# Performance work log

Measured on AMD Instinct MI355X. Metric: run time of the kernel, lower is better.

## Reference

```python
import jax, jax.numpy as jnp
import numpy as np

D_MODEL = 1280
N_HEADS = 16
DEPTH = D_MODEL // N_HEADS  # 80
NEG_BIG = -10000.0


def setup_inputs() -> dict:
    key = jax.random.key(0)
    ks = jax.random.split(key, 12)
    B, S = 2, 2048
    std = 1.0 / np.sqrt(D_MODEL)
    inp = {
        "v": jax.random.normal(ks[0], (B, S, D_MODEL), jnp.float32),
        "k": jax.random.normal(ks[1], (B, S, D_MODEL), jnp.float32),
        "q": jax.random.normal(ks[2], (B, S, D_MODEL), jnp.float32),
        # causal mask: 1.0 on strictly-upper triangle (future positions)
        "mask": jnp.triu(jnp.ones((S, S), jnp.float32), k=1),
        "Wq_w": jax.random.normal(ks[3], (D_MODEL, D_MODEL), jnp.float32) * std,
        "Wq_b": jnp.zeros((D_MODEL,), jnp.float32),
        "Wk_w": jax.random.normal(ks[4], (D_MODEL, D_MODEL), jnp.float32) * std,
        "Wk_b": jnp.zeros((D_MODEL,), jnp.float32),
        "Wv_w": jax.random.normal(ks[5], (D_MODEL, D_MODEL), jnp.float32) * std,
        "Wv_b": jnp.zeros((D_MODEL,), jnp.float32),
        "dense_w": jax.random.normal(ks[6], (D_MODEL, D_MODEL), jnp.float32) * std,
        "dense_b": jnp.zeros((D_MODEL,), jnp.float32),
    }
    return inp


def _split_heads(x, B):
    # [B, S, D] -> [B, H, S, depth]
    return x.reshape(B, -1, N_HEADS, DEPTH).transpose(0, 2, 1, 3)


def reference(v, k, q, mask, Wq_w, Wq_b, Wk_w, Wk_b, Wv_w, Wv_b, dense_w, dense_b):
    B = q.shape[0]
    # torch Linear: y = x @ W.T + b
    qh = _split_heads(q @ Wq_w.T + Wq_b, B)
    kh = _split_heads(k @ Wk_w.T + Wk_b, B)
    vh = _split_heads(v @ Wv_w.T + Wv_b, B)

    scale = 1.0 / np.sqrt(DEPTH)
    logits = jnp.einsum("bhqd,bhkd->bhqk", qh, kh) * scale  # [B,H,S,S]
    nd, ns = logits.shape[-2], logits.shape[-1]
    logits = logits + mask[ns - nd:ns, :ns] * NEG_BIG
    attn = jax.nn.softmax(logits, axis=-1)
    out = jnp.einsum("bhqk,bhkd->bhqd", attn, vh)  # [B,H,S,depth]
    out = out.transpose(0, 2, 1, 3).reshape(B, -1, D_MODEL)
    out = out @ dense_w.T + dense_b
    return out, attn
```

## Files before the change

### kernel.cpp

```cpp
#include <hip/hip_runtime.h>
#include <hip/hip_bf16.h>

typedef short frag8 __attribute__((ext_vector_type(8)));
typedef float facc4 __attribute__((ext_vector_type(4)));
typedef float f32x4 __attribute__((ext_vector_type(4)));
typedef unsigned short ushort_t;
typedef unsigned int uint_t;

#define DEV static __device__ __forceinline__

DEV ushort_t f2bf(float f) {
  uint_t u = __float_as_uint(f);
  u += 0x7fffu + ((u >> 16) & 1u);
  return (ushort_t)(u >> 16);
}
DEV uint_t cvt_pk(float lo, float hi) {
  uint_t r;
  asm("v_cvt_pk_bf16_f32 %0, %1, %2" : "=v"(r) : "v"(lo), "v"(hi));
  return r;
}
DEV frag8 pack8(float4 a, float4 b) {
  union { frag8 f; uint4 u; } u_;
  u_.u.x = cvt_pk(a.x, a.y); u_.u.y = cvt_pk(a.z, a.w);
  u_.u.z = cvt_pk(b.x, b.y); u_.u.w = cvt_pk(b.z, b.w);
  return u_.f;
}

constexpr int B_ = 2, S_ = 2048, H_ = 16, DM = 1280, DH = 80, DP = 96;
constexpr size_t IN_E = (size_t)B_ * S_ * DM;
constexpr size_t WT_E = (size_t)DM * DM;
constexpr size_t OFF_WQ = 0;
constexpr size_t OFF_WK = OFF_WQ + WT_E;
constexpr size_t OFF_WV = OFF_WK + WT_E;
constexpr size_t OFF_WD = OFF_WV + WT_E;
constexpr size_t QH_E  = (size_t)B_ * H_ * S_ * DP;
constexpr size_t OFF_QH = OFF_WD + WT_E;
constexpr size_t OFF_KH = OFF_QH + QH_E;
constexpr size_t VT_E  = (size_t)B_ * H_ * DH * S_;
constexpr size_t OFF_VT = OFF_KH + QH_E;
constexpr size_t OFF_OH = OFF_VT + VT_E;

constexpr float QSCALE = 0.16129822f;

__global__ void convert_kernel(const float* __restrict__ wq, const float* __restrict__ wk,
                               const float* __restrict__ wv, const float* __restrict__ wd,
                               ushort_t* __restrict__ ws) {
  size_t i = (size_t)blockIdx.x * blockDim.x + threadIdx.x;
  size_t stride = (size_t)gridDim.x * blockDim.x;
  constexpr size_t TOTAL = 4 * WT_E / 8;
  constexpr size_t NROW = (size_t)B_ * H_ * S_;
  constexpr size_t PADC = 2 * NROW * 2;
  for (size_t c = i; c < TOTAL + PADC; c += stride) {
    if (c < TOTAL) {
      size_t e = c * 8;
      const float* s2; size_t lo;
      if      (e < WT_E)     { s2 = wq; lo = e; }
      else if (e < 2 * WT_E) { s2 = wk; lo = e - WT_E; }
      else if (e < 3 * WT_E) { s2 = wv; lo = e - 2 * WT_E; }
      else                   { s2 = wd; lo = e - 3 * WT_E; }
      float4 a = *(const float4*)(s2 + lo);
      float4 b = *(const float4*)(s2 + lo + 4);
      uint4 o;
      o.x = (uint_t)f2bf(a.x) | ((uint_t)f2bf(a.y) << 16);
      o.y = (uint_t)f2bf(a.z) | ((uint_t)f2bf(a.w) << 16);
      o.z = (uint_t)f2bf(b.x) | ((uint_t)f2bf(b.y) << 16);
      o.w = (uint_t)f2bf(b.z) | ((uint_t)f2bf(b.w) << 16);
      *(uint4*)(ws + e) = o;
    } else {
      size_t rr = c - TOTAL;
      size_t row = rr >> 1;
      size_t base = (row < NROW ? OFF_QH : OFF_KH) + (row & (NROW - 1)) * DP + DH + (rr & 1) * 8;
      uint4 z = {0u, 0u, 0u, 0u};
      *(uint4*)(ws + base) = z;
    }
  }
}

__global__ __launch_bounds__(256) void qkv_kernel(const float* __restrict__ Aq,
                                                  const float* __restrict__ Ak,
                                                  const float* __restrict__ Av,
                                                  const ushort_t* __restrict__ wts,
                                                  const float* __restrict__ bq,
                                                  const float* __restrict__ bk,
                                                  const float* __restrict__ bv,
                                                  ushort_t* __restrict__ qh_o,
                                                  ushort_t* __restrict__ kh_o,
                                                  ushort_t* __restrict__ vt_o) {
  __shared__ __align__(16) ushort_t sA[2][128][40];
  __shared__ __align__(16) ushort_t sB[2][128][40];
  int which = blockIdx.x / 320;
  int local = blockIdx.x - which * 320;
  int swz = (local & 7) * 40 + (local >> 3);
  int tm = swz / 10, tn = swz % 10;
  int m0 = tm * 128, n0 = tn * 128;
  const float* A = which == 0 ? Aq : which == 1 ? Ak : Av;
  const ushort_t* W = wts + (size_t)which * WT_E;
  const float* bias = which == 0 ? bq : which == 1 ? bk : bv;
  int tid = threadIdx.x, l = tid & 63, wv = tid >> 6;
  int lm = l & 15, lg = l >> 4;
  int wr = wv >> 1, wc = wv & 1;
  int srow = tid >> 2, schk = tid & 3;
  facc4 acc[4][4] = {};
  frag8 ra[2], rb[2];

  auto load_tile = [&](int kt) {
    const float* Ab = A + (size_t)(m0 + srow) * DM + kt * 32 + schk * 8;
    ra[0] = pack8(*(const float4*)Ab, *(const float4*)(Ab + 4));
    const float* Ab2 = Ab + (size_t)64 * DM;
    ra[1] = pack8(*(const float4*)Ab2, *(const float4*)(Ab2 + 4));
    const ushort_t* Bb = W + (size_t)(n0 + srow) * DM + kt * 32 + schk * 8;
    rb[0] = *(const frag8*)Bb;
    rb[1] = *(const frag8*)(Bb + (size_t)64 * DM);
  };
  auto store_tile = [&](int bb) {
    *(frag8*)&sA[bb][srow][schk * 8] = ra[0];
    *(frag8*)&sA[bb][srow + 64][schk * 8] = ra[1];
    *(frag8*)&sB[bb][srow][schk * 8] = rb[0];
    *(frag8*)&sB[bb][srow + 64][schk * 8] = rb[1];
  };

  load_tile(0);
  store_tile(0);
  __syncthreads();
  for (int kt = 0; kt < 40; ++kt) {
    int cur = kt & 1;
    if (kt < 39) load_tile(kt + 1);
    frag8 af[4], bf[4];
#pragma unroll
    for (int i = 0; i < 4; ++i) af[i] = *(const frag8*)&sA[cur][wr * 64 + i * 16 + lm][lg * 8];
#pragma unroll
    for (int i = 0; i < 4; ++i) bf[i] = *(const frag8*)&sB[cur][wc * 64 + i * 16 + lm][lg * 8];
#pragma unroll
    for (int mi = 0; mi < 4; ++mi)
#pragma unroll
      for (int ni = 0; ni < 4; ++ni)
        acc[mi][ni] = __builtin_amdgcn_mfma_f32_16x16x32_bf16(af[mi], bf[ni], acc[mi][ni], 0, 0, 0);
    if (kt < 39) store_tile(cur ^ 1);
    __syncthreads();
  }

  float scale = (which == 0) ? QSCALE : 1.0f;
  ushort_t* dst = which == 0 ? qh_o : which == 1 ? kh_o : vt_o;
#pragma unroll
  for (int ni = 0; ni < 4; ++ni) {
    int n = n0 + wc * 64 + ni * 16 + lm;
    float bv2 = bias[n];
    int h = n / 80, d = n % 80;
#pragma unroll
    for (int mi = 0; mi < 4; ++mi) {
      int mbase = m0 + wr * 64 + mi * 16 + lg * 4;
      int b = mbase >> 11, sp = mbase & 2047;
      if (which < 2) {
#pragma unroll
        for (int r = 0; r < 4; ++r) {
          float vl = (acc[mi][ni][r] + bv2) * scale;
          dst[((size_t)(b * H_ + h) * S_ + sp + r) * DP + d] = f2bf(vl);
        }
      } else {
        uint2 u2;
        u2.x = cvt_pk(acc[mi][ni][0] + bv2, acc[mi][ni][1] + bv2);
        u2.y = cvt_pk(acc[mi][ni][2] + bv2, acc[mi][ni][3] + bv2);
        *(uint2*)&dst[((size_t)(b * H_ + h) * DH + d) * S_ + sp] = u2;
      }
    }
  }
}

__global__ __launch_bounds__(256) void dense_kernel(const ushort_t* __restrict__ A,
                                                    const ushort_t* __restrict__ W,
                                                    const float* __restrict__ bias,
                                                    float* __restrict__ dst_f) {
  __shared__ __align__(16) ushort_t sA[2][128][40];
  __shared__ __align__(16) ushort_t sB[2][128][40];
  int bid = blockIdx.x;
  int swz = (bid & 7) * 40 + (bid >> 3);
  int tm = swz / 10, tn = swz % 10;
  int m0 = tm * 128, n0 = tn * 128;
  int tid = threadIdx.x, l = tid & 63, wv = tid >> 6;
  int lm = l & 15, lg = l >> 4;
  int wr = wv >> 1, wc = wv & 1;
  int srow = tid >> 2, schk = tid & 3;
  facc4 acc[4][4] = {};
  frag8 ra[2], rb[2];

  auto load_tile = [&](int kt) {
    const ushort_t* Ab = A + (size_t)(m0 + srow) * DM + kt * 32 + schk * 8;
    ra[0] = *(const frag8*)Ab;
    ra[1] = *(const frag8*)(Ab + (size_t)64 * DM);
    const ushort_t* Bb = W + (size_t)(n0 + srow) * DM + kt * 32 + schk * 8;
    rb[0] = *(const frag8*)Bb;
    rb[1] = *(const frag8*)(Bb + (size_t)64 * DM);
  };
  auto store_tile = [&](int bb) {
    *(frag8*)&sA[bb][srow][schk * 8] = ra[0];
    *(frag8*)&sA[bb][srow + 64][schk * 8] = ra[1];
    *(frag8*)&sB[bb][srow][schk * 8] = rb[0];
    *(frag8*)&sB[bb][srow + 64][schk * 8] = rb[1];
  };

  load_tile(0);
  store_tile(0);
  __syncthreads();
  for (int kt = 0; kt < 40; ++kt) {
    int cur = kt & 1;
    if (kt < 39) load_tile(kt + 1);
    frag8 af[4], bf[4];
#pragma unroll
    for (int i = 0; i < 4; ++i) af[i] = *(const frag8*)&sA[cur][wr * 64 + i * 16 + lm][lg * 8];
#pragma unroll
    for (int i = 0; i < 4; ++i) bf[i] = *(const frag8*)&sB[cur][wc * 64 + i * 16 + lm][lg * 8];
#pragma unroll
    for (int mi = 0; mi < 4; ++mi)
#pragma unroll
      for (int ni = 0; ni < 4; ++ni)
        acc[mi][ni] = __builtin_amdgcn_mfma_f32_16x16x32_bf16(af[mi], bf[ni], acc[mi][ni], 0, 0, 0);
    if (kt < 39) store_tile(cur ^ 1);
    __syncthreads();
  }

#pragma unroll
  for (int ni = 0; ni < 4; ++ni) {
    int n = n0 + wc * 64 + ni * 16 + lm;
    float bv2 = bias[n];
#pragma unroll
    for (int mi = 0; mi < 4; ++mi) {
      int mbase = m0 + wr * 64 + mi * 16 + lg * 4;
#pragma unroll
      for (int r = 0; r < 4; ++r)
        __builtin_nontemporal_store(acc[mi][ni][r] + bv2, dst_f + (size_t)(mbase + r) * DM + n);
    }
  }
}

__global__ __launch_bounds__(512, 2) void attn_kernel(const ushort_t* __restrict__ qh,
                                                      const ushort_t* __restrict__ kh,
                                                      const ushort_t* __restrict__ vt,
                                                      ushort_t* __restrict__ outh,
                                                      float* __restrict__ out_attn) {
  __shared__ __align__(16) ushort_t sK[2][64][104];
  __shared__ __align__(16) char sP[8 * 2048];
  int bid = blockIdx.x;
  int half = bid >> 8, rr0 = bid & 255;
  int swz = (rr0 & 7) * 32 + (rr0 >> 3);
  int bh = swz >> 3, pr = swz & 7;
  int b = bh >> 4, h = bh & 15;
  int s = half ? (15 - pr) : pr;
  int tid = threadIdx.x, w = tid >> 6, l = tid & 63, lm = l & 15, lg = l >> 4;
  const ushort_t* qhb = qh + (size_t)bh * S_ * DP;
  const ushort_t* khb = kh + (size_t)bh * S_ * DP;
  const ushort_t* vtb = vt + (size_t)bh * DH * S_;
  float* attnb = out_attn + (size_t)bh * S_ * S_;
  char* Pw = sP + w * 2048;

  int sr[3], sc[3];
#pragma unroll
  for (int i = 0; i < 3; ++i) {
    int c = tid * 3 + i;
    sr[i] = c / 24; sc[i] = (c % 24) * 4;
  }
  uint2 st[3];
  auto ldt = [&](int t) {
#pragma unroll
    for (int i = 0; i < 3; ++i)
      st[i] = *(const uint2*)(khb + (size_t)(t * 64 + sr[i]) * DP + sc[i]);
  };
  auto stt = [&](int bb) {
#pragma unroll
    for (int i = 0; i < 3; ++i)
      *(uint2*)&sK[bb][sr[i]][sc[i]] = st[i];
  };

  int q0 = s * 128;
  int wq0 = q0 + w * 16;
  int qg = wq0 + lm;

  if (s < 15) {
    int c0 = (s + 1) * 128;
    int r2 = tid >> 2;
    int l4 = (tid & 3) << 2;
    float* rowp = attnb + (size_t)(q0 + r2) * S_ + c0 + l4;
    f32x4 z = {0.f, 0.f, 0.f, 0.f};
    for (int cc = 0; cc < 2048 - c0; cc += 16)
      __builtin_nontemporal_store(z, (f32x4*)(rowp + cc));
  }

  frag8 qf[3];
#pragma unroll
  for (int kd = 0; kd < 3; ++kd)
    qf[kd] = *(const frag8*)(qhb + (size_t)qg * DP + kd * 32 + lg * 8);
  int NT = 2 * (s + 1);

  float rs4[4] = {0.f, 0.f, 0.f, 0.f};
  ldt(0); stt(0); __syncthreads();
  for (int t = 0; t < NT; ++t) {
    int cur = t & 1;
    if (t + 1 < NT) ldt(t + 1);
    bool dead = (64 * t >= wq0 + 16);
    if (!dead) {
      facc4 acc[4] = {};
#pragma unroll
      for (int mi = 0; mi < 4; ++mi)
#pragma unroll
        for (int kd = 0; kd < 3; ++kd) {
          frag8 af = *(const frag8*)((const char*)sK + cur * (64 * 104 * 2) +
                                     (mi * 16 + lm) * 208 + kd * 64 + lg * 16);
          acc[mi] = __builtin_amdgcn_mfma_f32_16x16x32_bf16(af, qf[kd], acc[mi], 0, 0, 0);
        }
      if (64 * t + 63 <= wq0) {
#pragma unroll
        for (int mi = 0; mi < 4; ++mi)
#pragma unroll
          for (int r = 0; r < 4; ++r) rs4[r] += exp2f(acc[mi][r]);
      } else {
#pragma unroll
        for (int mi = 0; mi < 4; ++mi)
#pragma unroll
          for (int r = 0; r < 4; ++r) {
            int kg = t * 64 + mi * 16 + lg * 4 + r;
            if (kg <= qg) rs4[r] += exp2f(acc[mi][r]);
          }
      }
    }
    if (t + 1 < NT) stt(cur ^ 1);
    __syncthreads();
  }
  float rs = (rs4[0] + rs4[1]) + (rs4[2] + rs4[3]);
  rs += __shfl_xor(rs, 16);
  rs += __shfl_xor(rs, 32);
  float li = -__log2f(rs);

  facc4 acc2[5] = {};
  ldt(0); stt(0); __syncthreads();
  for (int t = 0; t < NT; ++t) {
    int cur = t & 1;
    if (t + 1 < NT) ldt(t + 1);
    bool dead = (64 * t >= wq0 + 16);
    if (dead) {
      f32x4 z = {0.f, 0.f, 0.f, 0.f};
#pragma unroll
      for (int mi = 0; mi < 4; ++mi)
        __builtin_nontemporal_store(z, (f32x4*)(attnb + (size_t)qg * S_ + t * 64 + mi * 16 + lg * 4));
    } else {
      facc4 acc[4] = {};
#pragma unroll
      for (int mi = 0; mi < 4; ++mi)
#pragma unroll
        for (int kd = 0; kd < 3; ++kd) {
          frag8 af = *(const frag8*)((const char*)sK + cur * (64 * 104 * 2) +
                                     (mi * 16 + lm) * 208 + kd * 64 + lg * 16);
          acc[mi] = __builtin_amdgcn_mfma_f32_16x16x32_bf16(af, qf[kd], acc[mi], 0, 0, 0);
        }
      bool full = (64 * t + 63 <= wq0);
#pragma unroll
      for (int mi = 0; mi < 4; ++mi) {
        float p[4];
        if (full) {
#pragma unroll
          for (int r = 0; r < 4; ++r) p[r] = exp2f(acc[mi][r] + li);
        } else {
#pragma unroll
          for (int r = 0; r < 4; ++r) {
            int kg = t * 64 + mi * 16 + lg * 4 + r;
            p[r] = (kg <= qg) ? exp2f(acc[mi][r] + li) : 0.f;
          }
        }
        f32x4 f4 = {p[0], p[1], p[2], p[3]};
        __builtin_nontemporal_store(f4, (f32x4*)(attnb + (size_t)qg * S_ + t * 64 + mi * 16 + lg * 4));
        uint2 pk;
        pk.x = cvt_pk(p[0], p[1]);
        pk.y = cvt_pk(p[2], p[3]);
        int kb = mi * 32 + lg * 8;
        *(uint2*)(Pw + lm * 128 + (kb ^ ((lm & 7) << 4))) = pk;
      }
#pragma unroll
      for (int ks = 0; ks < 2; ++ks) {
        int kbyte = ks * 64 + lg * 16;
        frag8 pa = *(const frag8*)(Pw + lm * 128 + (kbyte ^ ((lm & 7) << 4)));
#pragma unroll
        for (int nf = 0; nf < 5; ++nf) {
          frag8 vb = *(const frag8*)(vtb + (size_t)(nf * 16 + lm) * S_ + t * 64 + ks * 32 + lg * 8);
          acc2[nf] = __builtin_amdgcn_mfma_f32_16x16x32_bf16(pa, vb, acc2[nf], 0, 0, 0);
        }
      }
    }
    if (t + 1 < NT) stt(cur ^ 1);
    __syncthreads();
  }
#pragma unroll
  for (int nf = 0; nf < 5; ++nf)
#pragma unroll
    for (int r = 0; r < 4; ++r) {
      int qrow = q0 + w * 16 + lg * 4 + r;
      int col = h * DH + nf * 16 + lm;
      outh[((size_t)b * S_ + qrow) * DM + col] = f2bf(acc2[nf][r]);
    }
}

extern "C" void kernel_launch(void* const* d_in, const int* in_sizes, int n_in,
                              void* d_out, int out_size, void* d_ws, size_t ws_size,
                              hipStream_t stream) {
  const float* v  = (const float*)d_in[0];
  const float* k  = (const float*)d_in[1];
  const float* q  = (const float*)d_in[2];
  const float* wq = (const float*)d_in[4];
  const float* bq = (const float*)d_in[5];
  const float* wk = (const float*)d_in[6];
  const float* bk = (const float*)d_in[7];
  const float* wv = (const float*)d_in[8];
  const float* bv = (const float*)d_in[9];
  const float* wd = (const float*)d_in[10];
  const float* bd = (const float*)d_in[11];
  ushort_t* ws = (ushort_t*)d_ws;
  float* out  = (float*)d_out;
  float* attn = out + IN_E;

  convert_kernel<<<2048, 256, 0, stream>>>(wq, wk, wv, wd, ws);
  qkv_kernel<<<960, 256, 0, stream>>>(q, k, v, ws + OFF_WQ, bq, bk, bv,
                                      ws + OFF_QH, ws + OFF_KH, ws + OFF_VT);
  attn_kernel<<<512, 512, 0, stream>>>(ws + OFF_QH, ws + OFF_KH, ws + OFF_VT, ws + OFF_OH, attn);
  dense_kernel<<<320, 256, 0, stream>>>(ws + OFF_OH, ws + OFF_WD, bd, out);
}
```

Measured before the change: 352.0 us.

## Give each attention wave two 16-row query groups to reuse K and V fragments

The attention block drops from 8 to 4 waves, and each wave now handles 32 query rows as two 16-row groups. Each K tile fragment read from LDS and each V fragment read from global memory then feeds two MFMAs instead of one. K tile staging switches to 16-byte loads, and the block barriers are replaced by a custom waitcnt-plus-barrier. The cost is more registers per wave (two sets of accumulators and P values) and fewer waves per block to hide latency. Masked-row handling also becomes coarser, since compute is skipped only when both groups are fully dead.

```diff
diff --git a/kernel.cpp b/kernel.cpp
--- a/kernel.cpp
+++ b/kernel.cpp
@@ -25,6 +25,7 @@
   u_.u.z = cvt_pk(b.x, b.y); u_.u.w = cvt_pk(b.z, b.w);
   return u_.f;
 }
+DEV void bar_lds() { asm volatile("s_waitcnt lgkmcnt(0)\n\ts_barrier" ::: "memory"); }
 
 constexpr int B_ = 2, S_ = 2048, H_ = 16, DM = 1280, DH = 80, DP = 96;
 constexpr size_t IN_E = (size_t)B_ * S_ * DM;
@@ -232,13 +233,13 @@
   }
 }
 
-__global__ __launch_bounds__(512, 2) void attn_kernel(const ushort_t* __restrict__ qh,
+__global__ __launch_bounds__(256, 2) void attn_kernel(const ushort_t* __restrict__ qh,
                                                       const ushort_t* __restrict__ kh,
                                                       const ushort_t* __restrict__ vt,
                                                       ushort_t* __restrict__ outh,
                                                       float* __restrict__ out_attn) {
   __shared__ __align__(16) ushort_t sK[2][64][104];
-  __shared__ __align__(16) char sP[8 * 2048];
+  __shared__ __align__(16) char sP[4 * 4096];
   int bid = blockIdx.x;
   int half = bid >> 8, rr0 = bid & 255;
   int swz = (rr0 & 7) * 32 + (rr0 >> 3);
@@ -250,150 +251,193 @@
   const ushort_t* khb = kh + (size_t)bh * S_ * DP;
   const ushort_t* vtb = vt + (size_t)bh * DH * S_;
   float* attnb = out_attn + (size_t)bh * S_ * S_;
-  char* Pw = sP + w * 2048;
+  char* Pw = sP + w * 4096;
 
   int sr[3], sc[3];
 #pragma unroll
   for (int i = 0; i < 3; ++i) {
     int c = tid * 3 + i;
-    sr[i] = c / 24; sc[i] = (c % 24) * 4;
-  }
-  uint2 st[3];
+    sr[i] = c / 12; sc[i] = (c % 12) * 8;
+  }
+  uint4 st[3];
   auto ldt = [&](int t) {
 #pragma unroll
     for (int i = 0; i < 3; ++i)
-      st[i] = *(const uint2*)(khb + (size_t)(t * 64 + sr[i]) * DP + sc[i]);
+      st[i] = *(const uint4*)(khb + (size_t)(t * 64 + sr[i]) * DP + sc[i]);
   };
   auto stt = [&](int bb) {
 #pragma unroll
     for (int i = 0; i < 3; ++i)
-      *(uint2*)&sK[bb][sr[i]][sc[i]] = st[i];
+      *(uint4*)&sK[bb][sr[i]][sc[i]] = st[i];
   };
 
   int q0 = s * 128;
-  int wq0 = q0 + w * 16;
-  int qg = wq0 + lm;
+  int wq0 = q0 + w * 32;
 
   if (s < 15) {
     int c0 = (s + 1) * 128;
-    int r2 = tid >> 2;
-    int l4 = (tid & 3) << 2;
+    int r2 = tid >> 1;
+    int l4 = (tid & 1) << 2;
     float* rowp = attnb + (size_t)(q0 + r2) * S_ + c0 + l4;
     f32x4 z = {0.f, 0.f, 0.f, 0.f};
-    for (int cc = 0; cc < 2048 - c0; cc += 16)
+    for (int cc = 0; cc < 2048 - c0; cc += 8)
       __builtin_nontemporal_store(z, (f32x4*)(rowp + cc));
   }
 
-  frag8 qf[3];
-#pragma unroll
-  for (int kd = 0; kd < 3; ++kd)
-    qf[kd] = *(const frag8*)(qhb + (size_t)qg * DP + kd * 32 + lg * 8);
+  frag8 qf[2][3];
+#pragma unroll
+  for (int g = 0; g < 2; ++g)
+#pragma unroll
+    for (int kd = 0; kd < 3; ++kd)
+      qf[g][kd] = *(const frag8*)(qhb + (size_t)(wq0 + g * 16 + lm) * DP + kd * 32 + lg * 8);
   int NT = 2 * (s + 1);
 
-  float rs4[4] = {0.f, 0.f, 0.f, 0.f};
-  ldt(0); stt(0); __syncthreads();
+  float rs4[2][4] = {};
+  ldt(0); stt(0); bar_lds();
   for (int t = 0; t < NT; ++t) {
     int cur = t & 1;
     if (t + 1 < NT) ldt(t + 1);
-    bool dead = (64 * t >= wq0 + 16);
-    if (!dead) {
-      facc4 acc[4] = {};
+    if (64 * t < wq0 + 32) {
+      facc4 acc[2][4] = {};
 #pragma unroll
       for (int mi = 0; mi < 4; ++mi)
 #pragma unroll
         for (int kd = 0; kd < 3; ++kd) {
           frag8 af = *(const frag8*)((const char*)sK + cur * (64 * 104 * 2) +
                                      (mi * 16 + lm) * 208 + kd * 64 + lg * 16);
-          acc[mi] = __builtin_amdgcn_mfma_f32_16x16x32_bf16(af, qf[kd], acc[mi], 0, 0, 0);
-        }
-      if (64 * t + 63 <= wq0) {
-#pragma unroll
-        for (int mi = 0; mi < 4; ++mi)
-#pragma unroll
-          for (int r = 0; r < 4; ++r) rs4[r] += exp2f(acc[mi][r]);
-      } else {
-#pragma unroll
-        for (int mi = 0; mi < 4; ++mi)
-#pragma unroll
-          for (int r = 0; r < 4; ++r) {
-            int kg = t * 64 + mi * 16 + lg * 4 + r;
-            if (kg <= qg) rs4[r] += exp2f(acc[mi][r]);
-          }
+#pragma unroll
+          for (int g = 0; g < 2; ++g)
+            acc[g][mi] = __builtin_amdgcn_mfma_f32_16x16x32_bf16(af, qf[g][kd], acc[g][mi], 0, 0, 0);
+        }
+#pragma unroll
+      for (int g = 0; g < 2; ++g) {
+        int gq0 = wq0 + g * 16;
+        if (64 * t >= gq0 + 16) continue;
+        if (64 * t + 63 <= gq0) {
+#pragma unroll
+          for (int mi = 0; mi < 4; ++mi)
+#pragma unroll
+            for (int r = 0; r < 4; ++r) rs4[g][r] += exp2f(acc[g][mi][r]);
+        } else {
+          int qg = gq0 + lm;
+#pragma unroll
+          for (int mi = 0; mi < 4; ++mi)
+#pragma unroll
+            for (int r = 0; r < 4; ++r) {
+              int kg = t * 64 + mi * 16 + lg * 4 + r;
+              if (kg <= qg) rs4[g][r] += exp2f(acc[g][mi][r]);
+            }
+        }
       }
     }
     if (t + 1 < NT) stt(cur ^ 1);
-    __syncthreads();
-  }
-  float rs = (rs4[0] + rs4[1]) + (rs4[2] + rs4[3]);
-  rs += __shfl_xor(rs, 16);
-  rs += __shfl_xor(rs, 32);
-  float li = -__log2f(rs);
-
-  facc4 acc2[5] = {};
-  ldt(0); stt(0); __syncthreads();
+    bar_lds();
+  }
+  float li[2];
+#pragma unroll
+  for (int g = 0; g < 2; ++g) {
+    float rs = (rs4[g][0] + rs4[g][1]) + (rs4[g][2] + rs4[g][3]);
+    rs += __shfl_xor(rs, 16);
+    rs += __shfl_xor(rs, 32);
+    li[g] = -__log2f(rs);
+  }
+
+  facc4 acc2[2][5] = {};
+  ldt(0); stt(0); bar_lds();
   for (int t = 0; t < NT; ++t) {
     int cur = t & 1;
     if (t + 1 < NT) ldt(t + 1);
-    bool dead = (64 * t >= wq0 + 16);
-    if (dead) {
+    if (64 * t >= wq0 + 32) {
       f32x4 z = {0.f, 0.f, 0.f, 0.f};
 #pragma unroll
-      for (int mi = 0; mi < 4; ++mi)
-        __builtin_nontemporal_store(z, (f32x4*)(attnb + (size_t)qg * S_ + t * 64 + mi * 16 + lg * 4));
+      for (int g = 0; g < 2; ++g)
+#pragma unroll
+        for (int mi = 0; mi < 4; ++mi)
+          __builtin_nontemporal_store(z, (f32x4*)(attnb + (size_t)(wq0 + g * 16 + lm) * S_ +
+                                                  t * 64 + mi * 16 + lg * 4));
     } else {
-      facc4 acc[4] = {};
+      facc4 acc[2][4] = {};
 #pragma unroll
       for (int mi = 0; mi < 4; ++mi)
 #pragma unroll
         for (int kd = 0; kd < 3; ++kd) {
           frag8 af = *(const frag8*)((const char*)sK + cur * (64 * 104 * 2) +
                                      (mi * 16 + lm) * 208 + kd * 64 + lg * 16);
-          acc[mi] = __builtin_amdgcn_mfma_f32_16x16x32_bf16(af, qf[kd], acc[mi], 0, 0, 0);
-        }
-      bool full = (64 * t + 63 <= wq0);
-#pragma unroll
-      for (int mi = 0; mi < 4; ++mi) {
-        float p[4];
-        if (full) {
-#pragma unroll
-          for (int r = 0; r < 4; ++r) p[r] = exp2f(acc[mi][r] + li);
+#pragma unroll
+          for (int g = 0; g < 2; ++g)
+            acc[g][mi] = __builtin_amdgcn_mfma_f32_16x16x32_bf16(af, qf[g][kd], acc[g][mi], 0, 0, 0);
+        }
+      float pv[2][4][4];
+#pragma unroll
+      for (int g = 0; g < 2; ++g) {
+        int gq0 = wq0 + g * 16;
+        int qg = gq0 + lm;
+        if (64 * t >= gq0 + 16) {
+#pragma unroll
+          for (int mi = 0; mi < 4; ++mi)
+#pragma unroll
+            for (int r = 0; r < 4; ++r) pv[g][mi][r] = 0.f;
+        } else if (64 * t + 63 <= gq0) {
+#pragma unroll
+          for (int mi = 0; mi < 4; ++mi)
+#pragma unroll
+            for (int r = 0; r < 4; ++r) pv[g][mi][r] = exp2f(acc[g][mi][r] + li[g]);
         } else {
 #pragma unroll
-          for (int r = 0; r < 4; ++r) {
-            int kg = t * 64 + mi * 16 + lg * 4 + r;
-            p[r] = (kg <= qg) ? exp2f(acc[mi][r] + li) : 0.f;
-          }
-        }
-        f32x4 f4 = {p[0], p[1], p[2], p[3]};
-        __builtin_nontemporal_store(f4, (f32x4*)(attnb + (size_t)qg * S_ + t * 64 + mi * 16 + lg * 4));
-        uint2 pk;
-        pk.x = cvt_pk(p[0], p[1]);
-        pk.y = cvt_pk(p[2], p[3]);
-        int kb = mi * 32 + lg * 8;
-        *(uint2*)(Pw + lm * 128 + (kb ^ ((lm & 7) << 4))) = pk;
+          for (int mi = 0; mi < 4; ++mi)
+#pragma unroll
+            for (int r = 0; r < 4; ++r) {
+              int kg = t * 64 + mi * 16 + lg * 4 + r;
+              pv[g][mi][r] = (kg <= qg) ? exp2f(acc[g][mi][r] + li[g]) : 0.f;
+            }
+        }
+#pragma unroll
+        for (int mi = 0; mi < 4; ++mi) {
+          uint2 pk;
+          pk.x = cvt_pk(pv[g][mi][0], pv[g][mi][1]);
+          pk.y = cvt_pk(pv[g][mi][2], pv[g][mi][3]);
+          int kb = mi * 32 + lg * 8;
+          *(uint2*)(Pw + g * 2048 + lm * 128 + (kb ^ ((lm & 7) << 4))) = pk;
+        }
       }
 #pragma unroll
       for (int ks = 0; ks < 2; ++ks) {
         int kbyte = ks * 64 + lg * 16;
-        frag8 pa = *(const frag8*)(Pw + lm * 128 + (kbyte ^ ((lm & 7) << 4)));
+        frag8 pa[2];
+#pragma unroll
+        for (int g = 0; g < 2; ++g)
+          pa[g] = *(const frag8*)(Pw + g * 2048 + lm * 128 + (kbyte ^ ((lm & 7) << 4)));
 #pragma unroll
         for (int nf = 0; nf < 5; ++nf) {
           frag8 vb = *(const frag8*)(vtb + (size_t)(nf * 16 + lm) * S_ + t * 64 + ks * 32 + lg * 8);
-          acc2[nf] = __builtin_amdgcn_mfma_f32_16x16x32_bf16(pa, vb, acc2[nf], 0, 0, 0);
+#pragma unroll
+          for (int g = 0; g < 2; ++g)
+            acc2[g][nf] = __builtin_amdgcn_mfma_f32_16x16x32_bf16(pa[g], vb, acc2[g][nf], 0, 0, 0);
+        }
+      }
+#pragma unroll
+      for (int g = 0; g < 2; ++g) {
+        int qg = wq0 + g * 16 + lm;
+#pragma unroll
+        for (int mi = 0; mi < 4; ++mi) {
+          f32x4 f4 = {pv[g][mi][0], pv[g][mi][1], pv[g][mi][2], pv[g][mi][3]};
+          __builtin_nontemporal_store(f4, (f32x4*)(attnb + (size_t)qg * S_ + t * 64 + mi * 16 + lg * 4));
         }
       }
     }
     if (t + 1 < NT) stt(cur ^ 1);
-    __syncthreads();
-  }
-#pragma unroll
-  for (int nf = 0; nf < 5; ++nf)
-#pragma unroll
-    for (int r = 0; r < 4; ++r) {
-      int qrow = q0 + w * 16 + lg * 4 + r;
-      int col = h * DH + nf * 16 + lm;
-      outh[((size_t)b * S_ + qrow) * DM + col] = f2bf(acc2[nf][r]);
-    }
+    bar_lds();
+  }
+#pragma unroll
+  for (int g = 0; g < 2; ++g)
+#pragma unroll
+    for (int nf = 0; nf < 5; ++nf)
+#pragma unroll
+      for (int r = 0; r < 4; ++r) {
+        int qrow = q0 + w * 32 + g * 16 + lg * 4 + r;
+        int col = h * DH + nf * 16 + lm;
+        outh[((size_t)b * S_ + qrow) * DM + col] = f2bf(acc2[g][nf][r]);
+      }
 }
 
 extern "C" void kernel_launch(void* const* d_in, const int* in_sizes, int n_in,
@@ -417,6 +461,6 @@
   convert_kernel<<<2048, 256, 0, stream>>>(wq, wk, wv, wd, ws);
   qkv_kernel<<<960, 256, 0, stream>>>(q, k, v, ws + OFF_WQ, bq, bk, bv,
                                       ws + OFF_QH, ws + OFF_KH, ws + OFF_VT);
-  attn_kernel<<<512, 512, 0, stream>>>(ws + OFF_QH, ws + OFF_KH, ws + OFF_VT, ws + OFF_OH, attn);
+  attn_kernel<<<512, 256, 0, stream>>>(ws + OFF_QH, ws + OFF_KH, ws + OFF_VT, ws + OFF_OH, attn);
   dense_kernel<<<320, 256, 0, stream>>>(ws + OFF_OH, ws + OFF_WD, bd, out);
 }
```

New measurement: 713.7 us. +102.8%, slower.

## Stage V tiles in LDS with two-deep prefetch and lighter barriers in attention

Applied to the files above, without the earlier changes.

The attention kernel now stages V^T tiles in shared memory alongside K instead of reading them from global memory per MFMA fragment. Global loads for K and V are issued two tiles ahead, and the barrier is replaced by a custom lgkmcnt wait plus s_barrier. Launch bounds move to 4 blocks per CU and the attention-probability stores change from nontemporal to regular stores. The intent is fewer redundant global V reads and better load latency hiding, at the cost of extra LDS, more live registers, and a tighter register budget from the raised occupancy target.

```diff
diff --git a/kernel.cpp b/kernel.cpp
--- a/kernel.cpp
+++ b/kernel.cpp
@@ -25,6 +25,7 @@
   u_.u.z = cvt_pk(b.x, b.y); u_.u.w = cvt_pk(b.z, b.w);
   return u_.f;
 }
+DEV void bar_lds() { asm volatile("s_waitcnt lgkmcnt(0)\n\ts_barrier" ::: "memory"); }
 
 constexpr int B_ = 2, S_ = 2048, H_ = 16, DM = 1280, DH = 80, DP = 96;
 constexpr size_t IN_E = (size_t)B_ * S_ * DM;
@@ -232,12 +233,13 @@
   }
 }
 
-__global__ __launch_bounds__(512, 2) void attn_kernel(const ushort_t* __restrict__ qh,
+__global__ __launch_bounds__(512, 4) void attn_kernel(const ushort_t* __restrict__ qh,
                                                       const ushort_t* __restrict__ kh,
                                                       const ushort_t* __restrict__ vt,
                                                       ushort_t* __restrict__ outh,
                                                       float* __restrict__ out_attn) {
   __shared__ __align__(16) ushort_t sK[2][64][104];
+  __shared__ __align__(16) ushort_t sV[2][80][68];
   __shared__ __align__(16) char sP[8 * 2048];
   int bid = blockIdx.x;
   int half = bid >> 8, rr0 = bid & 255;
@@ -258,16 +260,26 @@
     int c = tid * 3 + i;
     sr[i] = c / 24; sc[i] = (c % 24) * 4;
   }
-  uint2 st[3];
-  auto ldt = [&](int t) {
+  uint2 stk[3];
+  auto ldtK = [&](int t) {
 #pragma unroll
     for (int i = 0; i < 3; ++i)
-      st[i] = *(const uint2*)(khb + (size_t)(t * 64 + sr[i]) * DP + sc[i]);
-  };
-  auto stt = [&](int bb) {
+      stk[i] = *(const uint2*)(khb + (size_t)(t * 64 + sr[i]) * DP + sc[i]);
+  };
+  auto sttK = [&](int bb) {
 #pragma unroll
     for (int i = 0; i < 3; ++i)
-      *(uint2*)&sK[bb][sr[i]][sc[i]] = st[i];
+      *(uint2*)&sK[bb][sr[i]][sc[i]] = stk[i];
+  };
+  int vrow = tid >> 3, vcol = (tid & 7) * 8;
+  uint4 stv0, stv1;
+  auto ldtV = [&](int t) {
+    stv0 = *(const uint4*)(vtb + (size_t)vrow * S_ + t * 64 + vcol);
+    if (tid < 128) stv1 = *(const uint4*)(vtb + (size_t)(64 + vrow) * S_ + t * 64 + vcol);
+  };
+  auto sttV = [&](int bb) {
+    *(uint4*)&sV[bb][vrow][vcol] = stv0;
+    if (tid < 128) *(uint4*)&sV[bb][64 + vrow][vcol] = stv1;
   };
 
   int q0 = s * 128;
@@ -291,12 +303,14 @@
   int NT = 2 * (s + 1);
 
   float rs4[4] = {0.f, 0.f, 0.f, 0.f};
-  ldt(0); stt(0); __syncthreads();
+  ldtK(0); sttK(0);
+  if (NT > 1) ldtK(1);
+  bar_lds();
   for (int t = 0; t < NT; ++t) {
     int cur = t & 1;
-    if (t + 1 < NT) ldt(t + 1);
-    bool dead = (64 * t >= wq0 + 16);
-    if (!dead) {
+    if (t + 1 < NT) sttK(cur ^ 1);
+    if (t + 2 < NT) ldtK(t + 2);
+    if (64 * t < wq0 + 16) {
       facc4 acc[4] = {};
 #pragma unroll
       for (int mi = 0; mi < 4; ++mi)
@@ -321,8 +335,7 @@
           }
       }
     }
-    if (t + 1 < NT) stt(cur ^ 1);
-    __syncthreads();
+    bar_lds();
   }
   float rs = (rs4[0] + rs4[1]) + (rs4[2] + rs4[3]);
   rs += __shfl_xor(rs, 16);
@@ -330,16 +343,18 @@
   float li = -__log2f(rs);
 
   facc4 acc2[5] = {};
-  ldt(0); stt(0); __syncthreads();
+  ldtK(0); ldtV(0); sttK(0); sttV(0);
+  if (NT > 1) { ldtK(1); ldtV(1); }
+  bar_lds();
   for (int t = 0; t < NT; ++t) {
     int cur = t & 1;
-    if (t + 1 < NT) ldt(t + 1);
-    bool dead = (64 * t >= wq0 + 16);
-    if (dead) {
+    if (t + 1 < NT) { sttK(cur ^ 1); sttV(cur ^ 1); }
+    if (t + 2 < NT) { ldtK(t + 2); ldtV(t + 2); }
+    if (64 * t >= wq0 + 16) {
       f32x4 z = {0.f, 0.f, 0.f, 0.f};
 #pragma unroll
       for (int mi = 0; mi < 4; ++mi)
-        __builtin_nontemporal_store(z, (f32x4*)(attnb + (size_t)qg * S_ + t * 64 + mi * 16 + lg * 4));
+        *(f32x4*)(attnb + (size_t)qg * S_ + t * 64 + mi * 16 + lg * 4) = z;
     } else {
       facc4 acc[4] = {};
 #pragma unroll
@@ -365,7 +380,7 @@
           }
         }
         f32x4 f4 = {p[0], p[1], p[2], p[3]};
-        __builtin_nontemporal_store(f4, (f32x4*)(attnb + (size_t)qg * S_ + t * 64 + mi * 16 + lg * 4));
+        *(f32x4*)(attnb + (size_t)qg * S_ + t * 64 + mi * 16 + lg * 4) = f4;
         uint2 pk;
         pk.x = cvt_pk(p[0], p[1]);
         pk.y = cvt_pk(p[2], p[3]);
@@ -378,13 +393,12 @@
         frag8 pa = *(const frag8*)(Pw + lm * 128 + (kbyte ^ ((lm & 7) << 4)));
 #pragma unroll
         for (int nf = 0; nf < 5; ++nf) {
-          frag8 vb = *(const frag8*)(vtb + (size_t)(nf * 16 + lm) * S_ + t * 64 + ks * 32 + lg * 8);
+          frag8 vb = *(const frag8*)&sV[cur][nf * 16 + lm][ks * 32 + lg * 8];
           acc2[nf] = __builtin_amdgcn_mfma_f32_16x16x32_bf16(pa, vb, acc2[nf], 0, 0, 0);
         }
       }
     }
-    if (t + 1 < NT) stt(cur ^ 1);
-    __syncthreads();
+    bar_lds();
   }
 #pragma unroll
   for (int nf = 0; nf < 5; ++nf)
```

New measurement: 353.2 us. Within noise of the previous version (+0.3%).
